# Kernel tuning notes

Measured on AMD Instinct MI355X. Metric: run time of the kernel, lower is better.

The kernel has to match this reference:

```python
import jax, jax.numpy as jnp
import numpy as np

V, E, HID, K, S = 100000, 256, 512, 20, 4096
HD = HID // 2  # per-direction LSTM hidden
START_ID, STOP_ID = 18, 19


def setup_inputs() -> dict:
    key = jax.random.key(0)
    ks = jax.random.split(key, 14)
    sentence = jax.random.randint(ks[0], (S,), 0, V)
    tags = jax.random.randint(ks[1], (S,), 0, START_ID)  # real tags only
    embed = jax.random.normal(ks[2], (V, E), jnp.float32) * 0.1
    w_ih_f = jax.random.normal(ks[3], (4 * HD, E), jnp.float32) * 0.05
    w_hh_f = jax.random.normal(ks[4], (4 * HD, HD), jnp.float32) * 0.05
    b_f = jax.random.normal(ks[5], (4 * HD,), jnp.float32) * 0.05
    w_ih_b = jax.random.normal(ks[6], (4 * HD, E), jnp.float32) * 0.05
    w_hh_b = jax.random.normal(ks[7], (4 * HD, HD), jnp.float32) * 0.05
    b_b = jax.random.normal(ks[8], (4 * HD,), jnp.float32) * 0.05
    h0 = jax.random.normal(ks[9], (2, HD), jnp.float32)
    c0 = jax.random.normal(ks[10], (2, HD), jnp.float32)
    emit_W = jax.random.normal(ks[11], (K, HID), jnp.float32) * 0.05
    emit_b = jax.random.normal(ks[12], (K,), jnp.float32) * 0.05
    transition = jax.random.normal(ks[13], (K, K), jnp.float32)
    transition = transition.at[START_ID, :].set(-10000.0)
    transition = transition.at[:, STOP_ID].set(-10000.0)
    return dict(sentence=sentence, tags=tags, embed=embed,
                w_ih_f=w_ih_f, w_hh_f=w_hh_f, b_f=b_f,
                w_ih_b=w_ih_b, w_hh_b=w_hh_b, b_b=b_b,
                h0=h0, c0=c0, emit_W=emit_W, emit_b=emit_b,
                transition=transition)


def _lstm_scan(xs, w_ih, w_hh, b, h, c):
    # xs: (S, E); torch gate order i, f, g, o
    def step(carry, x):
        h, c = carry
        z = x @ w_ih.T + h @ w_hh.T + b  # (4*HD,)
        i, f, g, o = jnp.split(z, 4)
        i, f, o = jax.nn.sigmoid(i), jax.nn.sigmoid(f), jax.nn.sigmoid(o)
        g = jnp.tanh(g)
        c = f * c + i * g
        h = o * jnp.tanh(c)
        return (h, c), h
    _, hs = jax.lax.scan(step, (h, c), xs)
    return hs  # (S, HD)


def reference(sentence, tags, embed, w_ih_f, w_hh_f, b_f,
              w_ih_b, w_hh_b, b_b, h0, c0, emit_W, emit_b, transition):
    xs = embed[sentence]  # (S, E)
    h_fwd = _lstm_scan(xs, w_ih_f, w_hh_f, b_f, h0[0], c0[0])
    h_bwd = _lstm_scan(xs[::-1], w_ih_b, w_hh_b, b_b, h0[1], c0[1])[::-1]
    feats = jnp.concatenate([h_fwd, h_bwd], axis=-1) @ emit_W.T + emit_b  # (S, K)

    # CRF forward algorithm (log-partition), tag dim fully vectorized.
    init_fv = jnp.full((K,), -10000.0, feats.dtype).at[START_ID].set(0.0)

    def crf_step(fv, feat):
        # fv_new[next] = logsumexp_prev(fv[prev] + T[next, prev] + feat[next])
        fv = jax.scipy.special.logsumexp(fv[None, :] + transition + feat[:, None], axis=1)
        return fv, None

    fv, _ = jax.lax.scan(crf_step, init_fv, feats)
    log_z = jax.scipy.special.logsumexp(fv + transition[STOP_ID])

    # Gold path score.
    tags_ext = jnp.concatenate([jnp.array([START_ID], tags.dtype), tags])
    gold = (transition[tags_ext[1:], tags_ext[:-1]].sum()
            + feats[jnp.arange(S), tags].sum()
            + transition[STOP_ID, tags[-1]])
    return jnp.stack([log_z, gold])
```

## Files before the change

kernel.cpp:

```cpp
#include <hip/hip_runtime.h>
#include <stdint.h>

#define SLEN 4096
#define EDIM 256
#define HD 256
#define G4 1024
#define KT 20
#define START_ID 18
#define STOP_ID 19

#define NVC 23
#define NLC 9
#define LSTM_LDS_BYTES (1024 + 1024 * NLC * 16)

typedef _Float16 half_t;
typedef _Float16 half2_t __attribute__((ext_vector_type(2)));

__device__ __forceinline__ float dot2(uint32_t w, uint32_t h, float acc) {
#if __has_builtin(__builtin_amdgcn_fdot2)
    return __builtin_amdgcn_fdot2(__builtin_bit_cast(half2_t, w),
                                  __builtin_bit_cast(half2_t, h), acc, false);
#else
    half2_t wv = __builtin_bit_cast(half2_t, w);
    half2_t hv = __builtin_bit_cast(half2_t, h);
    acc += (float)wv.x * (float)hv.x;
    acc += (float)wv.y * (float)hv.y;
    return acc;
#endif
}

__device__ __forceinline__ float fsig(float x) { return 1.f / (1.f + __expf(-x)); }
__device__ __forceinline__ float ftanh(float x) { return 1.f - 2.f / (__expf(2.f * x) + 1.f); }


__global__ __launch_bounds__(256) void k_transpose_ih(const float* __restrict__ wf,
                                                      const float* __restrict__ wb,
                                                      float* __restrict__ wT) {
    __shared__ float tile[32][33];
    int d = blockIdx.z;
    const float* w = d ? wb : wf;
    int ob = blockIdx.x * 32;
    int eb = blockIdx.y * 32;
    int tx = threadIdx.x & 31, ty = threadIdx.x >> 5;
#pragma unroll
    for (int r = 0; r < 32; r += 8)
        tile[ty + r][tx] = w[(long)(ob + ty + r) * EDIM + eb + tx];
    __syncthreads();
    float* dst = wT + (long)d * EDIM * G4;
#pragma unroll
    for (int r = 0; r < 32; r += 8)
        dst[(long)(eb + ty + r) * G4 + ob + tx] = tile[tx][ty + r];
}

__global__ __launch_bounds__(1024) void k_pack_hh(const float* __restrict__ whf,
                                                  const float* __restrict__ whb,
                                                  uint32_t* __restrict__ wpack,
                                                  uint32_t* __restrict__ wtail) {
    int d = blockIdx.y;
    const float* W = d ? whb : whf;
    int t = threadIdx.x;
    int wv = t >> 6, l = t & 63;
    int j = (wv << 4) | (l & 15);
    int g = (l >> 4) & 3;
    int o = g * 256 + j;
    int bx = blockIdx.x;
    if (bx < 92) {
        int k = bx * 2;
        half2_t p = {(half_t)W[(long)o * HD + k], (half_t)W[(long)o * HD + k + 1]};
        wpack[(d * 92 + bx) * 1024 + t] = __builtin_bit_cast(uint32_t, p);
    } else {
        int cb = bx - 92;
        uint32_t q[4];
#pragma unroll
        for (int qq = 0; qq < 4; qq++) {
            int k = 2 * (92 + cb * 4 + qq);
            half2_t p = {(half_t)W[(long)o * HD + k], (half_t)W[(long)o * HD + k + 1]};
            q[qq] = __builtin_bit_cast(uint32_t, p);
        }
        uint4* dst = (uint4*)wtail;
        dst[(d * NLC + cb) * 1024 + t] = make_uint4(q[0], q[1], q[2], q[3]);
    }
}

__global__ __launch_bounds__(256) void k_zx(const int* __restrict__ sentence,
                                            const float* __restrict__ embed,
                                            const float* __restrict__ wT,
                                            const float* __restrict__ bf,
                                            const float* __restrict__ bb,
                                            float* __restrict__ zxp) {
    int d = blockIdx.y;
    int s0 = blockIdx.x * 16;
    const float* bias = d ? bb : bf;
    __shared__ float xbuf[16][EDIM];
    int tid = threadIdx.x;
    for (int r = 0; r < 16; r++) {
        int row = sentence[s0 + r];
        xbuf[r][tid] = embed[(long)row * EDIM + tid];
    }
    __syncthreads();
    const float* wTd = wT + (long)d * EDIM * G4;
    for (int og = 0; og < 4; og++) {
        float acc[16];
#pragma unroll
        for (int r = 0; r < 16; r++) acc[r] = 0.f;
        int o = og * 256 + tid;
        for (int e = 0; e < EDIM; e += 4) {
            float w0 = wTd[(long)(e + 0) * G4 + o];
            float w1 = wTd[(long)(e + 1) * G4 + o];
            float w2 = wTd[(long)(e + 2) * G4 + o];
            float w3 = wTd[(long)(e + 3) * G4 + o];
#pragma unroll
            for (int r = 0; r < 16; r++) {
                float4 x4 = *(const float4*)&xbuf[r][e];
                acc[r] += w0 * x4.x + w1 * x4.y + w2 * x4.z + w3 * x4.w;
            }
        }
        float bv = bias[o];
        int tB = ((tid >> 4) << 6) | (og << 4) | (tid & 15);
#pragma unroll
        for (int r = 0; r < 16; r++)
            zxp[(long)(d * SLEN + s0 + r) * G4 + tB] = acc[r] + bv;
    }
}

__global__ __launch_bounds__(1024, 4) void k_lstm(const float* __restrict__ zxp,
                                                  const uint32_t* __restrict__ wpack,
                                                  const uint4* __restrict__ wtail,
                                                  const float* __restrict__ h0,
                                                  const float* __restrict__ c0,
                                                  float* __restrict__ hs) {
    extern __shared__ char smem[];
    uint4* h2q = (uint4*)smem;
    half_t* h2h = (half_t*)smem;
    uint4* tail = (uint4*)(smem + 1024);

    int d = blockIdx.x;
    int t = threadIdx.x;
    int l = t & 63;
    int j = ((t >> 6) << 4) | (l & 15);

    uint32_t wreg[4 * NVC];
#pragma unroll
    for (int kk = 0; kk < 4 * NVC; kk++) wreg[kk] = wpack[(d * 92 + kk) * 1024 + t];

#pragma unroll
    for (int cb = 0; cb < NLC; cb++)
        tail[cb * 1024 + t] = wtail[(d * NLC + cb) * 1024 + t];

    float c = c0[d * HD + j];
    if (t < 128) {
        half2_t p = {(half_t)h0[d * HD + 2 * t], (half_t)h0[d * HD + 2 * t + 1]};
        ((uint32_t*)h2q)[t] = __builtin_bit_cast(uint32_t, p);
    }
    __syncthreads();

    const float* zxd = zxp + (long)d * SLEN * G4 + t;
    float* hsd = hs + (long)d * SLEN * HD + j;

    float zx_next = zxd[(long)(d ? SLEN - 1 : 0) * G4];

    for (int s = 0; s < SLEN; s++) {
        const int p = s & 1;
        float zx = zx_next;
        if (s + 1 < SLEN) {
            int sxn = d ? (SLEN - 2 - s) : (s + 1);
            zx_next = zxd[(long)sxn * G4];
        }
        const uint4* hq = h2q + p * 32;
        float acc0 = 0.f, acc1 = 0.f;
#pragma unroll
        for (int cc = 0; cc < NVC; cc++) {
            uint4 hv = hq[cc];
            acc0 = dot2(wreg[4 * cc + 0], hv.x, acc0);
            acc1 = dot2(wreg[4 * cc + 1], hv.y, acc1);
            acc0 = dot2(wreg[4 * cc + 2], hv.z, acc0);
            acc1 = dot2(wreg[4 * cc + 3], hv.w, acc1);
        }
#pragma unroll
        for (int cb = 0; cb < NLC; cb++) {
            uint4 tw = tail[cb * 1024 + t];
            uint4 hv = hq[NVC + cb];
            acc0 = dot2(tw.x, hv.x, acc0);
            acc1 = dot2(tw.y, hv.y, acc1);
            acc0 = dot2(tw.z, hv.z, acc0);
            acc1 = dot2(tw.w, hv.w, acc1);
        }
        float z = acc0 + acc1 + zx;
        int lj = l & 15;
        float zi = __shfl(z, lj, 64);
        float zf = __shfl(z, lj + 16, 64);
        float zg = __shfl(z, lj + 32, 64);
        float zo = __shfl(z, lj + 48, 64);
        float ig = fsig(zi), fg = fsig(zf), og = fsig(zo);
        float gg = ftanh(zg);
        c = fg * c + ig * gg;
        float hval = og * ftanh(c);
        if (l < 16) {
            int sx = d ? (SLEN - 1 - s) : s;
            hsd[(long)sx * HD] = hval;
            h2h[((p ^ 1) << 8) + j] = (half_t)hval;
        }
        __syncthreads();
    }
}

__global__ __launch_bounds__(192) void k_feats(const float* __restrict__ hs,
                                               const float* __restrict__ emitW,
                                               const float* __restrict__ emitb,
                                               float* __restrict__ feats) {
    __shared__ float wb[KT][516];
    __shared__ float hb[8][516];
    int tid = threadIdx.x;
    int s0 = blockIdx.x * 8;
    for (int idx = tid; idx < KT * 512; idx += 192) {
        wb[idx >> 9][idx & 511] = emitW[idx];
    }
    for (int idx = tid; idx < 8 * 512; idx += 192) {
        int sl = idx >> 9, jj = idx & 511;
        float v = (jj < 256) ? hs[(long)(s0 + sl) * HD + jj]
                             : hs[(long)(SLEN + s0 + sl) * HD + (jj - 256)];
        hb[sl][jj] = v;
    }
    __syncthreads();
    if (tid < 160) {
        int sl = tid / KT, k = tid % KT;
        float acc = emitb[k];
        for (int jj = 0; jj < 512; jj += 4) {
            float4 wv = *(const float4*)&wb[k][jj];
            float4 hv = *(const float4*)&hb[sl][jj];
            acc += wv.x * hv.x + wv.y * hv.y + wv.z * hv.z + wv.w * hv.w;
        }
        feats[(long)(s0 + sl) * KT + k] = acc;
    }
}

__global__ __launch_bounds__(256) void k_gold(const float* __restrict__ feats,
                                              const int* __restrict__ tags,
                                              const float* __restrict__ trans,
                                              float* __restrict__ out) {
    __shared__ float red[256];
    int tid = threadIdx.x;
    float local = 0.f;
    for (int s2 = tid; s2 < SLEN; s2 += 256) {
        int cur = tags[s2];
        int prev = s2 ? tags[s2 - 1] : START_ID;
        local += trans[cur * KT + prev] + feats[(long)s2 * KT + cur];
    }
    red[tid] = local;
    __syncthreads();
    for (int off = 128; off; off >>= 1) {
        if (tid < off) red[tid] += red[tid + off];
        __syncthreads();
    }
    if (tid == 0) out[1] = red[0] + trans[STOP_ID * KT + tags[SLEN - 1]];
}

__global__ __launch_bounds__(512) void k_crf_chunk(const float* __restrict__ feats,
                                                   const float* __restrict__ trans,
                                                   float* __restrict__ mats) {
    __shared__ float T[KT][KT + 1];
    __shared__ float fb[16][KT];
    __shared__ float cur[2][KT][KT + 1];
    int tid = threadIdx.x;
    int t0 = blockIdx.x * 16;
    if (tid < KT * KT) T[tid / KT][tid % KT] = trans[tid];
    for (int idx = tid; idx < 16 * KT; idx += 512) fb[idx / KT][idx % KT] = feats[(long)t0 * KT + idx];
    __syncthreads();
    int i = tid / KT, jc = tid % KT;
    bool act = tid < KT * KT;
    if (act) cur[0][i][jc] = T[i][jc] + fb[0][i];
    __syncthreads();
    for (int m = 1; m < 16; m++) {
        int p = (m - 1) & 1;
        float nv = 0.f;
        if (act) {
            float vs[KT], vmax = -1e30f;
#pragma unroll
            for (int k = 0; k < KT; k++) { vs[k] = T[i][k] + cur[p][k][jc]; vmax = fmaxf(vmax, vs[k]); }
            float sum = 0.f;
#pragma unroll
            for (int k = 0; k < KT; k++) sum += __expf(vs[k] - vmax);
            nv = fb[m][i] + vmax + __logf(sum);
        }
        if (act) cur[p ^ 1][i][jc] = nv;
        __syncthreads();
    }
    if (act) mats[(long)blockIdx.x * (KT * KT) + tid] = cur[1][i][jc];
}

__global__ __launch_bounds__(512) void k_crf_combine(const float* __restrict__ in,
                                                     float* __restrict__ out_mats,
                                                     int per_block,
                                                     const float* __restrict__ trans,
                                                     float* __restrict__ d_out_ptr,
                                                     int finalize) {
    __shared__ float A[KT][KT + 1];
    __shared__ float cur[2][KT][KT + 1];
    int tid = threadIdx.x;
    int b = blockIdx.x;
    int i = tid / KT, jc = tid % KT;
    bool act = tid < KT * KT;
    const float* base = in + (long)b * per_block * (KT * KT);
    if (act) cur[0][i][jc] = base[tid];
    __syncthreads();
    for (int m = 1; m < per_block; m++) {
        int p = (m - 1) & 1;
        if (act) A[i][jc] = base[(long)m * KT * KT + tid];
        __syncthreads();
        float nv = 0.f;
        if (act) {
            float vs[KT], vmax = -1e30f;
#pragma unroll
            for (int k = 0; k < KT; k++) { vs[k] = A[i][k] + cur[p][k][jc]; vmax = fmaxf(vmax, vs[k]); }
            float sum = 0.f;
#pragma unroll
            for (int k = 0; k < KT; k++) sum += __expf(vs[k] - vmax);
            nv = vmax + __logf(sum);
        }
        if (act) cur[p ^ 1][i][jc] = nv;
        __syncthreads();
    }
    int fbuf = (per_block - 1) & 1;
    if (!finalize) {
        if (act) out_mats[(long)b * KT * KT + tid] = cur[fbuf][i][jc];
        return;
    }
    if (tid == 0) {
        float fv[KT];
        for (int ii = 0; ii < KT; ii++) {
            float vs[KT], vmax = -1e30f;
            for (int k = 0; k < KT; k++) {
                float v = cur[fbuf][ii][k] + (k == START_ID ? 0.f : -10000.f);
                vs[k] = v;
                vmax = fmaxf(vmax, v);
            }
            float sum = 0.f;
            for (int k = 0; k < KT; k++) sum += __expf(vs[k] - vmax);
            fv[ii] = vmax + __logf(sum);
        }
        float vs2[KT], vmax = -1e30f;
        for (int ii = 0; ii < KT; ii++) {
            float v = fv[ii] + trans[STOP_ID * KT + ii];
            vs2[ii] = v;
            vmax = fmaxf(vmax, v);
        }
        float sum = 0.f;
        for (int ii = 0; ii < KT; ii++) sum += __expf(vs2[ii] - vmax);
        d_out_ptr[0] = vmax + __logf(sum);
    }
}

extern "C" void kernel_launch(void* const* d_in, const int* in_sizes, int n_in,
                              void* d_out, int out_size, void* d_ws, size_t ws_size,
                              hipStream_t stream) {
    const int* sentence = (const int*)d_in[0];
    const int* tags = (const int*)d_in[1];
    const float* embed = (const float*)d_in[2];
    const float* w_ih_f = (const float*)d_in[3];
    const float* w_hh_f = (const float*)d_in[4];
    const float* b_f = (const float*)d_in[5];
    const float* w_ih_b = (const float*)d_in[6];
    const float* w_hh_b = (const float*)d_in[7];
    const float* b_b = (const float*)d_in[8];
    const float* h0 = (const float*)d_in[9];
    const float* c0 = (const float*)d_in[10];
    const float* emit_W = (const float*)d_in[11];
    const float* emit_b = (const float*)d_in[12];
    const float* transition = (const float*)d_in[13];
    float* out = (float*)d_out;

    char* ws = (char*)d_ws;
    float* zxp = (float*)(ws + 0);
    float* hs = (float*)(ws + 33554432);
    float* wT = (float*)(ws + 41943040);
    uint32_t* wpack = (uint32_t*)(ws + 44040192);
    uint32_t* wtail = (uint32_t*)(ws + 44793856);
    float* feats = (float*)(ws + 45088768);
    float* mats = (float*)(ws + 45416448);
    float* mats2 = (float*)(ws + 45826048);

    (void)hipFuncSetAttribute((const void*)k_lstm,
                              hipFuncAttributeMaxDynamicSharedMemorySize,
                              LSTM_LDS_BYTES);

    k_transpose_ih<<<dim3(32, 8, 2), 256, 0, stream>>>(w_ih_f, w_ih_b, wT);
    k_pack_hh<<<dim3(101, 2), 1024, 0, stream>>>(w_hh_f, w_hh_b, wpack, wtail);
    k_zx<<<dim3(256, 2), 256, 0, stream>>>(sentence, embed, wT, b_f, b_b, zxp);
    k_lstm<<<dim3(2), 1024, LSTM_LDS_BYTES, stream>>>(zxp, wpack, (const uint4*)wtail, h0, c0, hs);
    k_feats<<<dim3(512), 192, 0, stream>>>(hs, emit_W, emit_b, feats);
    k_gold<<<dim3(1), 256, 0, stream>>>(feats, tags, transition, out);
    k_crf_chunk<<<dim3(256), 512, 0, stream>>>(feats, transition, mats);
    k_crf_combine<<<dim3(16), 512, 0, stream>>>(mats, mats2, 16, transition, out, 0);
    k_crf_combine<<<dim3(1), 512, 0, stream>>>(mats2, nullptr, 16, transition, out, 1);
}
```

Before: 9.015 ms.

## Split LSTM recurrence across four workgroups per direction with global flag sync

The sequential LSTM, previously one 1024-thread workgroup per direction, is split across four 512-thread workgroups per direction. Each holds its quarter of W_hh in registers, writes its hidden slice to a global buffer and publishes a per-step flag that its peers spin on. The h vector is now broadcast by wave shuffles instead of LDS, and the weight packing and zx layout are reordered to match the new mapping. The aim is to cut per-step matvec work and drop the LDS tail, at the cost of a cross-CU global round trip on every step. Correctness also depends on the four workgroups being resident at the same time.

```diff
diff --git a/kernel.cpp b/kernel.cpp
--- a/kernel.cpp
+++ b/kernel.cpp
@@ -8,10 +8,7 @@
 #define KT 20
 #define START_ID 18
 #define STOP_ID 19
-
-#define NVC 23
-#define NLC 9
-#define LSTM_LDS_BYTES (1024 + 1024 * NLC * 16)
+#define NCU 4
 
 typedef _Float16 half_t;
 typedef _Float16 half2_t __attribute__((ext_vector_type(2)));
@@ -52,34 +49,25 @@
         dst[(long)(eb + ty + r) * G4 + ob + tx] = tile[tx][ty + r];
 }
 
-__global__ __launch_bounds__(1024) void k_pack_hh(const float* __restrict__ whf,
-                                                  const float* __restrict__ whb,
-                                                  uint32_t* __restrict__ wpack,
-                                                  uint32_t* __restrict__ wtail) {
-    int d = blockIdx.y;
+__global__ __launch_bounds__(512) void k_pack_hh(const float* __restrict__ whf,
+                                                 const float* __restrict__ whb,
+                                                 uint32_t* __restrict__ wpack,
+                                                 int* __restrict__ flags) {
+    int m = blockIdx.x;
+    int by = blockIdx.y;
+    int d = by >> 2, cix = by & 3;
     const float* W = d ? whb : whf;
     int t = threadIdx.x;
-    int wv = t >> 6, l = t & 63;
-    int j = (wv << 4) | (l & 15);
-    int g = (l >> 4) & 3;
-    int o = g * 256 + j;
-    int bx = blockIdx.x;
-    if (bx < 92) {
-        int k = bx * 2;
-        half2_t p = {(half_t)W[(long)o * HD + k], (half_t)W[(long)o * HD + k + 1]};
-        wpack[(d * 92 + bx) * 1024 + t] = __builtin_bit_cast(uint32_t, p);
-    } else {
-        int cb = bx - 92;
-        uint32_t q[4];
-#pragma unroll
-        for (int qq = 0; qq < 4; qq++) {
-            int k = 2 * (92 + cb * 4 + qq);
-            half2_t p = {(half_t)W[(long)o * HD + k], (half_t)W[(long)o * HD + k + 1]};
-            q[qq] = __builtin_bit_cast(uint32_t, p);
-        }
-        uint4* dst = (uint4*)wtail;
-        dst[(d * NLC + cb) * 1024 + t] = make_uint4(q[0], q[1], q[2], q[3]);
-    }
+    int w = t >> 6, l = t & 63;
+    int q = l >> 4, rp = l & 15, ul = rp & 7, ga = rp >> 3;
+    int isB = m >> 5;
+    int g = 2 * isB + ga;
+    int row = g * 256 + 64 * cix + 8 * w + ul;
+    int j = 32 * q + (m & 31);
+    half2_t pk = {(half_t)W[(long)row * HD + 2 * j],
+                  (half_t)W[(long)row * HD + 2 * j + 1]};
+    wpack[((long)(d * NCU + cix) * 64 + m) * 512 + t] = __builtin_bit_cast(uint32_t, pk);
+    if (m == 0 && by == 0 && t < 2 * NCU) flags[t] = 0;
 }
 
 __global__ __launch_bounds__(256) void k_zx(const int* __restrict__ sentence,
@@ -116,91 +104,115 @@
             }
         }
         float bv = bias[o];
-        int tB = ((tid >> 4) << 6) | (og << 4) | (tid & 15);
+        int U = tid;
+        int slot = (((U >> 6) * 8 + ((U >> 3) & 7)) << 5) + (U & 7) + 8 * (og & 1) + 16 * (og >> 1);
 #pragma unroll
         for (int r = 0; r < 16; r++)
-            zxp[(long)(d * SLEN + s0 + r) * G4 + tB] = acc[r] + bv;
-    }
-}
-
-__global__ __launch_bounds__(1024, 4) void k_lstm(const float* __restrict__ zxp,
-                                                  const uint32_t* __restrict__ wpack,
-                                                  const uint4* __restrict__ wtail,
-                                                  const float* __restrict__ h0,
-                                                  const float* __restrict__ c0,
-                                                  float* __restrict__ hs) {
-    extern __shared__ char smem[];
-    uint4* h2q = (uint4*)smem;
-    half_t* h2h = (half_t*)smem;
-    uint4* tail = (uint4*)(smem + 1024);
-
-    int d = blockIdx.x;
+            zxp[(long)(d * SLEN + s0 + r) * G4 + slot] = acc[r] + bv;
+    }
+}
+
+__global__ __launch_bounds__(512) void k_lstm(const float* __restrict__ zxp,
+                                              const uint32_t* __restrict__ wpack,
+                                              const float* __restrict__ h0,
+                                              const float* __restrict__ c0,
+                                              float* __restrict__ hs,
+                                              float* hglob,
+                                              int* flags) {
+    int b = blockIdx.x;
+    int dir = b & 7;
+    if (dir >= 2) return;
+    int cix = b >> 3;
     int t = threadIdx.x;
-    int l = t & 63;
-    int j = ((t >> 6) << 4) | (l & 15);
-
-    uint32_t wreg[4 * NVC];
-#pragma unroll
-    for (int kk = 0; kk < 4 * NVC; kk++) wreg[kk] = wpack[(d * 92 + kk) * 1024 + t];
-
-#pragma unroll
-    for (int cb = 0; cb < NLC; cb++)
-        tail[cb * 1024 + t] = wtail[(d * NLC + cb) * 1024 + t];
-
-    float c = c0[d * HD + j];
-    if (t < 128) {
-        half2_t p = {(half_t)h0[d * HD + 2 * t], (half_t)h0[d * HD + 2 * t + 1]};
-        ((uint32_t*)h2q)[t] = __builtin_bit_cast(uint32_t, p);
-    }
-    __syncthreads();
-
-    const float* zxd = zxp + (long)d * SLEN * G4 + t;
-    float* hsd = hs + (long)d * SLEN * HD + j;
-
-    float zx_next = zxd[(long)(d ? SLEN - 1 : 0) * G4];
+    int w = t >> 6, l = t & 63;
+    int rp = l & 15, ul = rp & 7;
+    int U = 64 * cix + 8 * w + ul;
+
+    uint32_t wreg[64];
+    {
+        const uint32_t* wp = wpack + ((long)(dir * NCU + cix) * 64) * 512 + t;
+#pragma unroll
+        for (int m = 0; m < 64; m++) wreg[m] = wp[m * 512];
+#pragma unroll
+        for (int m = 0; m < 64; m++) asm volatile("" : "+v"(wreg[m]));
+    }
+
+    float cst = c0[dir * HD + U];
+
+    const float* zxd = zxp + (long)dir * SLEN * G4 + (cix * 8 + w) * 32;
+    float* hsd = hs + (long)dir * SLEN * HD;
+    float* hg = hglob + dir * 2 * HD;
+    int* flg = flags + dir * NCU;
+
+    int sx0 = dir ? (SLEN - 1) : 0;
+    float zxa_n = zxd[(long)sx0 * G4 + rp];
+    float zxb_n = zxd[(long)sx0 * G4 + rp + 16];
+
+    float f0 = h0[dir * HD + 4 * l + 0], f1 = h0[dir * HD + 4 * l + 1];
+    float f2 = h0[dir * HD + 4 * l + 2], f3 = h0[dir * HD + 4 * l + 3];
+
+    int srcbase = l & 48;
 
     for (int s = 0; s < SLEN; s++) {
-        const int p = s & 1;
-        float zx = zx_next;
+        int p2 = (s & 1) ^ 1;
+        float zxa = zxa_n, zxb = zxb_n;
         if (s + 1 < SLEN) {
-            int sxn = d ? (SLEN - 2 - s) : (s + 1);
-            zx_next = zxd[(long)sxn * G4];
-        }
-        const uint4* hq = h2q + p * 32;
-        float acc0 = 0.f, acc1 = 0.f;
-#pragma unroll
-        for (int cc = 0; cc < NVC; cc++) {
-            uint4 hv = hq[cc];
-            acc0 = dot2(wreg[4 * cc + 0], hv.x, acc0);
-            acc1 = dot2(wreg[4 * cc + 1], hv.y, acc1);
-            acc0 = dot2(wreg[4 * cc + 2], hv.z, acc0);
-            acc1 = dot2(wreg[4 * cc + 3], hv.w, acc1);
-        }
-#pragma unroll
-        for (int cb = 0; cb < NLC; cb++) {
-            uint4 tw = tail[cb * 1024 + t];
-            uint4 hv = hq[NVC + cb];
-            acc0 = dot2(tw.x, hv.x, acc0);
-            acc1 = dot2(tw.y, hv.y, acc1);
-            acc0 = dot2(tw.z, hv.z, acc0);
-            acc1 = dot2(tw.w, hv.w, acc1);
-        }
-        float z = acc0 + acc1 + zx;
-        int lj = l & 15;
-        float zi = __shfl(z, lj, 64);
-        float zf = __shfl(z, lj + 16, 64);
-        float zg = __shfl(z, lj + 32, 64);
-        float zo = __shfl(z, lj + 48, 64);
+            int sxn = dir ? (SLEN - 2 - s) : (s + 1);
+            zxa_n = zxd[(long)sxn * G4 + rp];
+            zxb_n = zxd[(long)sxn * G4 + rp + 16];
+        }
+        half2_t h01 = {(half_t)f0, (half_t)f1};
+        half2_t h23 = {(half_t)f2, (half_t)f3};
+        uint32_t hx = __builtin_bit_cast(uint32_t, h01);
+        uint32_t hy = __builtin_bit_cast(uint32_t, h23);
+
+        float za = 0.f, zb = 0.f;
+#pragma unroll
+        for (int mm = 0; mm < 16; mm++) {
+            uint32_t ha = (uint32_t)__shfl((int)hx, srcbase + mm, 64);
+            uint32_t hb = (uint32_t)__shfl((int)hy, srcbase + mm, 64);
+            za = dot2(wreg[2 * mm + 0], ha, za);
+            za = dot2(wreg[2 * mm + 1], hb, za);
+            zb = dot2(wreg[32 + 2 * mm + 0], ha, zb);
+            zb = dot2(wreg[32 + 2 * mm + 1], hb, zb);
+        }
+        za += __shfl_xor(za, 16, 64); za += __shfl_xor(za, 32, 64);
+        zb += __shfl_xor(zb, 16, 64); zb += __shfl_xor(zb, 32, 64);
+        za += zxa; zb += zxb;
+        float zi = __shfl(za, ul, 64);
+        float zf = __shfl(za, ul + 8, 64);
+        float zg = __shfl(zb, ul, 64);
+        float zo = __shfl(zb, ul + 8, 64);
         float ig = fsig(zi), fg = fsig(zf), og = fsig(zo);
         float gg = ftanh(zg);
-        c = fg * c + ig * gg;
-        float hval = og * ftanh(c);
-        if (l < 16) {
-            int sx = d ? (SLEN - 1 - s) : s;
-            hsd[(long)sx * HD] = hval;
-            h2h[((p ^ 1) << 8) + j] = (half_t)hval;
-        }
-        __syncthreads();
+        cst = fg * cst + ig * gg;
+        float hval = og * ftanh(cst);
+        if (l < 8) {
+            int sx = dir ? (SLEN - 1 - s) : s;
+            hsd[(long)sx * HD + U] = hval;
+            __hip_atomic_store(&hg[p2 * HD + U], hval,
+                               __ATOMIC_RELAXED, __HIP_MEMORY_SCOPE_AGENT);
+        }
+        __syncthreads();
+        if (t == 0) {
+            __hip_atomic_store(&flg[cix], s + 1,
+                               __ATOMIC_RELEASE, __HIP_MEMORY_SCOPE_AGENT);
+#pragma unroll
+            for (int pi = 0; pi < NCU - 1; pi++) {
+                int peer = pi + (pi >= cix ? 1 : 0);
+                while (__hip_atomic_load(&flg[peer], __ATOMIC_ACQUIRE,
+                                         __HIP_MEMORY_SCOPE_AGENT) <= s)
+                    __builtin_amdgcn_s_sleep(1);
+            }
+        }
+        __syncthreads();
+        if (s + 1 < SLEN) {
+            const float* src = &hg[p2 * HD + 4 * l];
+            f0 = __hip_atomic_load(src + 0, __ATOMIC_RELAXED, __HIP_MEMORY_SCOPE_AGENT);
+            f1 = __hip_atomic_load(src + 1, __ATOMIC_RELAXED, __HIP_MEMORY_SCOPE_AGENT);
+            f2 = __hip_atomic_load(src + 2, __ATOMIC_RELAXED, __HIP_MEMORY_SCOPE_AGENT);
+            f3 = __hip_atomic_load(src + 3, __ATOMIC_RELAXED, __HIP_MEMORY_SCOPE_AGENT);
+        }
     }
 }
 
@@ -374,19 +386,16 @@
     float* hs = (float*)(ws + 33554432);
     float* wT = (float*)(ws + 41943040);
     uint32_t* wpack = (uint32_t*)(ws + 44040192);
-    uint32_t* wtail = (uint32_t*)(ws + 44793856);
     float* feats = (float*)(ws + 45088768);
     float* mats = (float*)(ws + 45416448);
     float* mats2 = (float*)(ws + 45826048);
-
-    (void)hipFuncSetAttribute((const void*)k_lstm,
-                              hipFuncAttributeMaxDynamicSharedMemorySize,
-                              LSTM_LDS_BYTES);
+    float* hglob = (float*)(ws + 45851648);
+    int* flags = (int*)(ws + 45855744);
 
     k_transpose_ih<<<dim3(32, 8, 2), 256, 0, stream>>>(w_ih_f, w_ih_b, wT);
-    k_pack_hh<<<dim3(101, 2), 1024, 0, stream>>>(w_hh_f, w_hh_b, wpack, wtail);
+    k_pack_hh<<<dim3(64, 8), 512, 0, stream>>>(w_hh_f, w_hh_b, wpack, flags);
     k_zx<<<dim3(256, 2), 256, 0, stream>>>(sentence, embed, wT, b_f, b_b, zxp);
-    k_lstm<<<dim3(2), 1024, LSTM_LDS_BYTES, stream>>>(zxp, wpack, (const uint4*)wtail, h0, c0, hs);
+    k_lstm<<<dim3(32), 512, 0, stream>>>(zxp, wpack, h0, c0, hs, hglob, flags);
     k_feats<<<dim3(512), 192, 0, stream>>>(hs, emit_W, emit_b, feats);
     k_gold<<<dim3(1), 256, 0, stream>>>(feats, tags, transition, out);
     k_crf_chunk<<<dim3(256), 512, 0, stream>>>(feats, transition, mats);
```

New measurement: 14.99 ms. 1.66x slower.
